# Performance work log

Measured on AMD Instinct MI355X. Metric: run time of the kernel, lower is better.

## Reference

```python
import math
import jax, jax.numpy as jnp
import numpy as np

B, N, T, H, DIN, NH = 4, 256, 30, 128, 3, 8
BN = B * N
DH = H // NH


def _pos_embed(t, h):
    pos = np.arange(t)[:, None].astype(np.float64)
    div = np.exp(np.arange(0, h, 2) * (-math.log(10000.0) / h))
    pe = np.zeros((t, h), np.float32)
    pe[:, 0::2] = np.sin(pos * div)
    pe[:, 1::2] = np.cos(pos * div)
    return jnp.asarray(pe)


def setup_inputs() -> dict:
    key = jax.random.key(0)
    ks = jax.random.split(key, 24)
    lin = lambda k, i, o: (jax.random.normal(k, (i, o), jnp.float32) / np.sqrt(i).astype(np.float32))
    vec = lambda k, o: jax.random.normal(k, (o,), jnp.float32) * 0.02
    return dict(
        x_raw=jax.random.normal(ks[0], (T, BN, DIN), jnp.float32),
        adjacency=jax.random.bernoulli(ks[1], 0.01, (T, BN, BN)).astype(jnp.float32),
        ego_mask=jax.random.bernoulli(ks[2], 0.5, (B, T, N)),
        W1=lin(ks[3], DIN, H), b1=vec(ks[4], H),
        W2=lin(ks[5], H, H), b2=vec(ks[6], H),
        Wq=lin(ks[7], H, H), bq=vec(ks[8], H),
        Wk=lin(ks[9], H, H), bk=vec(ks[10], H),
        Wv=lin(ks[11], H, H), bv=vec(ks[12], H),
        Wqi=lin(ks[13], H, H), bqi=vec(ks[14], H),
        Wki=lin(ks[15], H, H), bki=vec(ks[16], H),
        Wvi=lin(ks[17], H, H), bvi=vec(ks[18], H),
        Wo=lin(ks[19], H, H), bo=vec(ks[20], H),
    )


def reference(x_raw, adjacency, ego_mask,
              W1, b1, W2, b2,
              Wq, bq, Wk, bk, Wv, bv,
              Wqi, bqi, Wki, bki, Wvi, bvi,
              Wo, bo):
    # (B,T,N) -> (T, B*N) node-active mask, matching permute(1,0,2).reshape
    mask_flat = ego_mask.transpose(1, 0, 2).reshape(T, BN).astype(x_raw.dtype)

    def step(_, inp):
        x_t, A_t, m = inp  # (BN,DIN), (BN,BN), (BN,)
        # mask rows/cols (equiv. to gather A[idx][:,idx]) and add self loops
        A = A_t * m[:, None] * m[None, :] + jnp.diag(m)
        deg = A.sum(axis=1)
        dinv = jnp.where(deg > 0, 1.0, 0.0) * jax.lax.rsqrt(jnp.where(deg > 0, deg, 1.0))
        An = dinv[:, None] * A * dinv[None, :]  # D^-1/2 (A+I) D^-1/2
        h1 = jax.nn.relu(An @ (x_t @ W1) + b1)
        h2 = jax.nn.relu(An @ (h1 @ W2) + b2) * m[:, None]  # scatter back into zeros
        return None, h2

    _, hs = jax.lax.scan(step, None, (x_raw, adjacency, mask_flat))  # (T,BN,H)

    x_seq = hs.transpose(1, 0, 2) + _pos_embed(T, H)  # (BN,T,H)
    Q = x_seq @ Wq + bq
    K = x_seq @ Wk + bk
    V = x_seq @ Wv + bv
    # nn.MultiheadAttention applies its own in-projection to Q/K/V
    q = (Q @ Wqi + bqi).reshape(BN, T, NH, DH)
    k = (K @ Wki + bki).reshape(BN, T, NH, DH)
    v = (V @ Wvi + bvi).reshape(BN, T, NH, DH)
    attn = jax.nn.softmax(jnp.einsum('bthd,bshd->bhts', q, k) / np.sqrt(DH).astype(np.float32), axis=-1)
    o = jnp.einsum('bhts,bshd->bthd', attn, v).reshape(BN, T, H)
    out = (o @ Wo + bo).reshape(B, N, T, H)
    return out
```

## Files before the change

kernel.cpp:

```cpp
#include <hip/hip_runtime.h>
#include <hip/hip_bf16.h>
#include <math.h>

#define TT  30
#define BNN 1024
#define HH  128
#define MT  (TT*BNN)
#define CAP 64

typedef short bf16x8 __attribute__((ext_vector_type(8)));
typedef float f32x4 __attribute__((ext_vector_type(4)));

__device__ __forceinline__ float ldf(const void* p, size_t i, int fp) {
  if (fp == 0) {
    unsigned int w = ((unsigned int)(((const unsigned short*)p)[i])) << 16;
    float f; __builtin_memcpy(&f, &w, 4); return f;
  }
  return ((const float*)p)[i];
}
__device__ __forceinline__ float bf2f(unsigned short u) {
  unsigned int w = ((unsigned int)u) << 16;
  float f; __builtin_memcpy(&f, &w, 4); return f;
}
__device__ __forceinline__ unsigned short f2bf(float f) {
  unsigned int u; __builtin_memcpy(&u, &f, 4);
  return (unsigned short)((u + 0x7FFFu + ((u >> 16) & 1u)) >> 16);
}
__device__ __forceinline__ void splitbf(float a, unsigned short& h, unsigned short& l) {
  h = f2bf(a);
  l = f2bf(a - bf2f(h));
}

__global__ __launch_bounds__(1024) void detect_kernel(const unsigned char* xb, const unsigned char* eb, int* mode) {
  __shared__ int cnt_exp, f3F_odd1, f3F_any, fnz_notm4;
  int tid = threadIdx.x;
  if (tid == 0) { cnt_exp = 0; f3F_odd1 = 0; f3F_any = 0; fnz_notm4 = 0; }
  __syncthreads();
  int local = 0;
  for (int i = tid; i < 2048; i += 1024) {
    int e = (((const unsigned short*)xb)[i] >> 8) & 0x7F;
    if (e >= 0x3A && e <= 0x41) local++;
  }
  atomicAdd(&cnt_exp, local);
  int l1 = 0, l2 = 0, l3 = 0;
  for (int i = tid; i < 7680; i += 1024) {
    unsigned int w = ((const unsigned int*)eb)[i];
    #pragma unroll
    for (int e = 0; e < 4; ++e) {
      unsigned char b = (w >> (8 * e)) & 0xff;
      if (b == 0x3F) { l2 = 1; if (e == 1) l1 = 1; }
      if (b != 0 && e != 0) l3 = 1;
    }
  }
  if (l1) atomicOr(&f3F_odd1, 1);
  if (l2) atomicOr(&f3F_any, 1);
  if (l3) atomicOr(&fnz_notm4, 1);
  __syncthreads();
  if (tid == 0) {
    mode[0] = (cnt_exp > 1536) ? 0 : 1;
    mode[1] = f3F_odd1 ? 0 : (f3F_any ? 1 : (fnz_notm4 ? 2 : 3));
  }
}

__global__ __launch_bounds__(256) void setup_kernel(
    const void* ego,
    const void* W1, const void* b1, const void* W2, const void* b2, const void* Wo, const void* bo,
    const void* Wq, const void* bq, const void* Wk, const void* bk, const void* Wv, const void* bv,
    const void* Wqi, const void* bqi, const void* Wki, const void* bki, const void* Wvi, const void* bvi,
    const int* mode, float* pe, float* W1f, float* b1f, float* b2f, float* bof,
    unsigned short* W2h, unsigned short* W2l, unsigned short* Woh, unsigned short* Wol,
    unsigned short* Wch, unsigned short* Wcl, float* bqkv, float* maskf) {
  int bid = blockIdx.x;
  int fp = mode[0];
  if (bid < 15) {
    int idx = bid * 256 + threadIdx.x;
    if (idx >= TT * HH) return;
    int t = idx >> 7, i = idx & 127, j = i >> 1;
    double div = exp((double)(2 * j) * (-log(10000.0) / 128.0));
    double ang = (double)t * div;
    pe[idx] = (i & 1) ? (float)cos(ang) : (float)sin(ang);
    return;
  }
  if (bid < 146) {
    int idx = (bid - 15) * 256 + threadIdx.x;
    if (idx < 16384) { int k = idx >> 7, h = idx & 127; splitbf(ldf(W2, idx, fp), W2h[h * 128 + k], W2l[h * 128 + k]); return; }
    idx -= 16384;
    if (idx < 16384) { int k = idx >> 7, h = idx & 127; splitbf(ldf(Wo, idx, fp), Woh[h * 128 + k], Wol[h * 128 + k]); return; }
    idx -= 16384;
    if (idx < 384) { W1f[idx] = ldf(W1, idx, fp); return; } idx -= 384;
    if (idx < 128) { b1f[idx] = ldf(b1, idx, fp); return; } idx -= 128;
    if (idx < 128) { b2f[idx] = ldf(b2, idx, fp); return; } idx -= 128;
    if (idx < 128) { bof[idx] = ldf(bo, idx, fp); return; }
    return;
  }
  if (bid < 266) {
    int idx = (bid - 146) * 256 + threadIdx.x;
    if (idx >= MT) return;
    int t = idx >> 10, p = idx & 1023, b = p >> 8, n = p & 255;
    size_t e = (size_t)b * (TT * 256) + (size_t)t * 256 + n;
    int mm = mode[1];
    bool nz;
    if      (mm == 0) nz = ((const unsigned short*)ego)[e] != 0;
    else if (mm == 1) nz = ((const float*)ego)[e] != 0.f;
    else if (mm == 2) nz = ((const unsigned char*)ego)[e] != 0;
    else              nz = ((const int*)ego)[e] != 0;
    maskf[idx] = nz ? 1.f : 0.f;
    return;
  }
  int cb = bid - 266;
  int g = cb / 65;
  const void* Wa = (g == 0) ? Wq : (g == 1) ? Wk : Wv;
  const void* ba = (g == 0) ? bq : (g == 1) ? bk : bv;
  const void* Wb = (g == 0) ? Wqi : (g == 1) ? Wki : Wvi;
  const void* bb = (g == 0) ? bqi : (g == 1) ? bki : bvi;
  unsigned short* Wh = Wch + (size_t)g * 16384;
  unsigned short* Wl = Wcl + (size_t)g * 16384;
  float* bc = bqkv + g * 128;
  int idx = (cb % 65) * 256 + threadIdx.x;
  if (idx < 16384) {
    int k = idx >> 7, h = idx & 127;
    float s = 0.f;
    #pragma unroll 8
    for (int m = 0; m < 128; ++m) s += ldf(Wa, k * 128 + m, fp) * ldf(Wb, m * 128 + h, fp);
    splitbf(s, Wh[h * 128 + k], Wl[h * 128 + k]);
  } else if (idx < 16512) {
    int h = idx - 16384;
    float s = ldf(bb, h, fp);
    #pragma unroll 8
    for (int m = 0; m < 128; ++m) s += ldf(ba, m, fp) * ldf(Wb, m * 128 + h, fp);
    bc[h] = s;
  }
}

__global__ __launch_bounds__(256) void csr_kernel(const void* A, const int* mode, const float* maskf,
                                                  int* nnz, int* cols, float* dinv) {
  int fp = mode[0];
  int r = blockIdx.x * 4 + (threadIdx.x >> 6);
  int lane = threadIdx.x & 63;
  int t = r >> 10, i = r & 1023;
  int tb = t << 10;
  if (maskf[r] == 0.f) { if (lane == 0) { nnz[r] = 0; dinv[r] = 0.f; } return; }
  int* myc = cols + (size_t)r * CAP;
  int cnt = 0;
  unsigned long long lmask = (1ull << lane) - 1ull;
  if (fp == 1) {
    const float* Ar = (const float*)A + (size_t)t * BNN * BNN + (size_t)i * BNN;
    #pragma unroll
    for (int it = 0; it < 4; ++it) {
      int j0 = it * 256 + lane * 4;
      float4 av = *(const float4*)(Ar + j0);
      float4 mv = *(const float4*)(maskf + tb + j0);
      float va[4] = {av.x * mv.x, av.y * mv.y, av.z * mv.z, av.w * mv.w};
      #pragma unroll
      for (int e = 0; e < 4; ++e) {
        bool hit = va[e] != 0.f;
        unsigned long long bal = __ballot(hit);
        if (hit) { int pos = cnt + __popcll(bal & lmask); if (pos < CAP) myc[pos] = j0 + e; }
        cnt += __popcll(bal);
      }
    }
  } else {
    const unsigned short* Ar = (const unsigned short*)A + (size_t)t * BNN * BNN + (size_t)i * BNN;
    #pragma unroll
    for (int it = 0; it < 2; ++it) {
      int j0 = it * 512 + lane * 8;
      uint4 av = *(const uint4*)(Ar + j0);
      unsigned int wv[4] = {av.x, av.y, av.z, av.w};
      float4 m0 = *(const float4*)(maskf + tb + j0);
      float4 m1 = *(const float4*)(maskf + tb + j0 + 4);
      float mm[8] = {m0.x, m0.y, m0.z, m0.w, m1.x, m1.y, m1.z, m1.w};
      #pragma unroll
      for (int e = 0; e < 8; ++e) {
        unsigned short u = (wv[e >> 1] >> ((e & 1) * 16)) & 0xffff;
        bool hit = (u != 0) && (mm[e] != 0.f);
        unsigned long long bal = __ballot(hit);
        if (hit) { int pos = cnt + __popcll(bal & lmask); if (pos < CAP) myc[pos] = j0 + e; }
        cnt += __popcll(bal);
      }
    }
  }
  if (lane == 0) { nnz[r] = cnt > CAP ? CAP : cnt; dinv[r] = rsqrtf((float)cnt + 1.0f); }
}

__global__ __launch_bounds__(256) void spmm1_kernel(const void* x, const int* mode, const int* nnz,
    const int* cols, const float* dinv, const float* W1f, const float* b1f, float* h1) {
  int fp = mode[0];
  int r = blockIdx.x * 4 + (threadIdx.x >> 6);
  int lane = threadIdx.x & 63;
  int tbase = (r >> 10) << 10;
  int n = nnz[r];
  float s0 = 0.f, s1 = 0.f, s2 = 0.f;
  int j = -1;
  if (lane < n) j = tbase + cols[(size_t)r * CAP + lane];
  else if (lane == n) j = r;
  if (j >= 0) {
    float dj = dinv[j];
    s0 = dj * ldf(x, (size_t)j * 3 + 0, fp);
    s1 = dj * ldf(x, (size_t)j * 3 + 1, fp);
    s2 = dj * ldf(x, (size_t)j * 3 + 2, fp);
  }
  #pragma unroll
  for (int d = 1; d < 64; d <<= 1) {
    s0 += __shfl_xor(s0, d);
    s1 += __shfl_xor(s1, d);
    s2 += __shfl_xor(s2, d);
  }
  float dr = dinv[r];
  #pragma unroll
  for (int u = 0; u < 2; ++u) {
    int h = lane + u * 64;
    float v = dr * (s0 * W1f[h] + s1 * W1f[128 + h] + s2 * W1f[256 + h]) + b1f[h];
    h1[(size_t)r * 128 + h] = fmaxf(v, 0.f);
  }
}

__global__ __launch_bounds__(256) void spmm2_kernel(const float* g2s, const int* nnz, const int* cols,
    const float* dinv, const float* b2f, const float* maskf, const float* pe, float* xseq) {
  int r = blockIdx.x * 4 + (threadIdx.x >> 6);
  int lane = threadIdx.x & 63;
  int c = lane * 2;
  int t = r >> 10, i = r & 1023;
  int n = nnz[r];
  const int* myc = cols + (size_t)r * CAP;
  const float* st = g2s + ((size_t)(t << 10)) * 128;
  float2 acc = *(const float2*)(g2s + (size_t)r * 128 + c);
  for (int s = 0; s < n; ++s) {
    float2 v = *(const float2*)(st + (size_t)myc[s] * 128 + c);
    acc.x += v.x; acc.y += v.y;
  }
  float dr = dinv[r], m = maskf[r];
  float2 b = *(const float2*)(b2f + c);
  float2 p = *(const float2*)(pe + t * 128 + c);
  float vx = fmaxf(dr * acc.x + b.x, 0.f) * m + p.x;
  float vy = fmaxf(dr * acc.y + b.y, 0.f) * m + p.y;
  *(float2*)(xseq + ((size_t)i * TT + t) * 128 + c) = make_float2(vx, vy);
}

__global__ __launch_bounds__(256) void mfma_gemm(const float* A, const unsigned short* Bhi,
    const unsigned short* Blo, const float* scale, const float* bias,
    float* outf, void* outfin, const int* mode) {
  __shared__ __align__(16) unsigned short Ah[64 * 64];
  __shared__ __align__(16) unsigned short Al[64 * 64];
  __shared__ __align__(16) unsigned short Bh[128 * 64];
  __shared__ __align__(16) unsigned short Bl[128 * 64];
  int tid = threadIdx.x;
  int rowTile = blockIdx.x * 64;
  int gy = blockIdx.y;
  const unsigned short* Bhp = Bhi + (size_t)gy * 16384;
  const unsigned short* Blp = Blo + (size_t)gy * 16384;
  const float* bp = bias ? (bias + gy * 128) : nullptr;
  float* ofp = outf ? (outf + (size_t)gy * ((size_t)MT * 128)) : nullptr;

  int lane = tid & 63;
  int wid = tid >> 6;
  int wrow = (wid >> 1) * 32, wcol = (wid & 1) * 64;
  f32x4 acc[2][4];
  #pragma unroll
  for (int m = 0; m < 2; ++m)
    #pragma unroll
    for (int n = 0; n < 4; ++n) acc[m][n] = (f32x4){0.f, 0.f, 0.f, 0.f};

  for (int kb = 0; kb < 2; ++kb) {
    __syncthreads();
    #pragma unroll
    for (int it = 0; it < 2; ++it) {
      int c = it * 256 + tid;
      int r = c >> 3, cc = c & 7;
      int swz = (cc ^ (r & 7)) * 16;
      const float* ap = A + (size_t)(rowTile + r) * 128 + kb * 64 + cc * 8;
      float4 f0 = *(const float4*)ap;
      float4 f1 = *(const float4*)(ap + 4);
      float fa[8] = {f0.x, f0.y, f0.z, f0.w, f1.x, f1.y, f1.z, f1.w};
      unsigned short hi[8], lo[8];
      #pragma unroll
      for (int e = 0; e < 8; ++e) splitbf(fa[e], hi[e], lo[e]);
      uint4 ph, pl;
      ph.x = hi[0] | ((unsigned)hi[1] << 16); ph.y = hi[2] | ((unsigned)hi[3] << 16);
      ph.z = hi[4] | ((unsigned)hi[5] << 16); ph.w = hi[6] | ((unsigned)hi[7] << 16);
      pl.x = lo[0] | ((unsigned)lo[1] << 16); pl.y = lo[2] | ((unsigned)lo[3] << 16);
      pl.z = lo[4] | ((unsigned)lo[5] << 16); pl.w = lo[6] | ((unsigned)lo[7] << 16);
      *(uint4*)((char*)Ah + r * 128 + swz) = ph;
      *(uint4*)((char*)Al + r * 128 + swz) = pl;
    }
    #pragma unroll
    for (int it = 0; it < 4; ++it) {
      int c = it * 256 + tid;
      int r = c >> 3, cc = c & 7;
      int swz = (cc ^ (r & 7)) * 16;
      *(uint4*)((char*)Bh + r * 128 + swz) = *(const uint4*)(Bhp + (size_t)r * 128 + kb * 64 + cc * 8);
      *(uint4*)((char*)Bl + r * 128 + swz) = *(const uint4*)(Blp + (size_t)r * 128 + kb * 64 + cc * 8);
    }
    __syncthreads();
    #pragma unroll
    for (int ks = 0; ks < 2; ++ks) {
      bf16x8 ah[2], al[2], bh[4], bl[4];
      #pragma unroll
      for (int m = 0; m < 2; ++m) {
        int R = wrow + m * 16 + (lane & 15);
        int cc = ks * 4 + (lane >> 4);
        int off = R * 128 + ((cc ^ (R & 7)) * 16);
        ah[m] = *(const bf16x8*)((const char*)Ah + off);
        al[m] = *(const bf16x8*)((const char*)Al + off);
      }
      #pragma unroll
      for (int n = 0; n < 4; ++n) {
        int R = wcol + n * 16 + (lane & 15);
        int cc = ks * 4 + (lane >> 4);
        int off = R * 128 + ((cc ^ (R & 7)) * 16);
        bh[n] = *(const bf16x8*)((const char*)Bh + off);
        bl[n] = *(const bf16x8*)((const char*)Bl + off);
      }
      #pragma unroll
      for (int m = 0; m < 2; ++m)
        #pragma unroll
        for (int n = 0; n < 4; ++n) {
          acc[m][n] = __builtin_amdgcn_mfma_f32_16x16x32_bf16(ah[m], bl[n], acc[m][n], 0, 0, 0);
          acc[m][n] = __builtin_amdgcn_mfma_f32_16x16x32_bf16(al[m], bh[n], acc[m][n], 0, 0, 0);
          acc[m][n] = __builtin_amdgcn_mfma_f32_16x16x32_bf16(ah[m], bh[n], acc[m][n], 0, 0, 0);
        }
    }
  }
  int fp = mode[0];
  #pragma unroll
  for (int m = 0; m < 2; ++m) {
    #pragma unroll
    for (int n = 0; n < 4; ++n) {
      int col = wcol + n * 16 + (lane & 15);
      float bv = bp ? bp[col] : 0.f;
      #pragma unroll
      for (int q = 0; q < 4; ++q) {
        int row = rowTile + wrow + m * 16 + (lane >> 4) * 4 + q;
        float v = acc[m][n][q];
        if (scale) v *= scale[row];
        v += bv;
        size_t o = (size_t)row * 128 + col;
        if (ofp)           ofp[o] = v;
        else if (fp == 0)  ((unsigned short*)outfin)[o] = f2bf(v);
        else               ((float*)outfin)[o] = v;
      }
    }
  }
}

__global__ __launch_bounds__(256) void attn_kernel(const float* Q, const float* K, const float* V, float* O) {
  __shared__ __align__(16) float ksm[TT * 128];
  __shared__ __align__(16) float vsm[TT * 128];
  int tid = threadIdx.x;
  size_t base = (size_t)blockIdx.x * (TT * 128);
  for (int i = tid; i < TT * 128 / 4; i += 256) {
    ((float4*)ksm)[i] = ((const float4*)(K + base))[i];
    ((float4*)vsm)[i] = ((const float4*)(V + base))[i];
  }
  int h = tid >> 5, t = tid & 31;
  float q[16];
  if (t < TT) {
    const float4* qp = (const float4*)(Q + base + (size_t)t * 128 + h * 16);
    #pragma unroll
    for (int e = 0; e < 4; ++e) { float4 f = qp[e]; q[4*e] = f.x; q[4*e+1] = f.y; q[4*e+2] = f.z; q[4*e+3] = f.w; }
  }
  __syncthreads();
  if (t >= TT) return;
  float p[TT];
  float mx = -1e30f;
  #pragma unroll
  for (int s = 0; s < TT; ++s) {
    const float4* kp = (const float4*)&ksm[s * 128 + h * 16];
    float d = 0.f;
    #pragma unroll
    for (int e = 0; e < 4; ++e) {
      float4 f = kp[e];
      d += q[4*e] * f.x + q[4*e+1] * f.y + q[4*e+2] * f.z + q[4*e+3] * f.w;
    }
    p[s] = d * 0.25f;
    mx = fmaxf(mx, p[s]);
  }
  float sum = 0.f;
  #pragma unroll
  for (int s = 0; s < TT; ++s) { p[s] = __expf(p[s] - mx); sum += p[s]; }
  float inv = 1.f / sum;
  float o[16];
  #pragma unroll
  for (int e = 0; e < 16; ++e) o[e] = 0.f;
  #pragma unroll
  for (int s = 0; s < TT; ++s) {
    const float4* vp = (const float4*)&vsm[s * 128 + h * 16];
    float ps = p[s] * inv;
    #pragma unroll
    for (int e = 0; e < 4; ++e) {
      float4 f = vp[e];
      o[4*e] += ps * f.x; o[4*e+1] += ps * f.y; o[4*e+2] += ps * f.z; o[4*e+3] += ps * f.w;
    }
  }
  float* op = O + base + (size_t)t * 128 + h * 16;
  #pragma unroll
  for (int e = 0; e < 4; ++e)
    ((float4*)op)[e] = make_float4(o[4*e], o[4*e+1], o[4*e+2], o[4*e+3]);
}

extern "C" void kernel_launch(void* const* d_in, const int* in_sizes, int n_in,
                              void* d_out, int out_size, void* d_ws, size_t ws_size,
                              hipStream_t stream) {
  (void)in_sizes; (void)n_in; (void)out_size;
  const void* x_raw = d_in[0];
  const void* adj   = d_in[1];
  const void* ego   = d_in[2];
  const void* W1 = d_in[3];  const void* b1 = d_in[4];
  const void* W2 = d_in[5];  const void* b2 = d_in[6];
  const void* Wq = d_in[7];  const void* bq = d_in[8];
  const void* Wk = d_in[9];  const void* bk = d_in[10];
  const void* Wv = d_in[11]; const void* bv = d_in[12];
  const void* Wqi = d_in[13]; const void* bqi = d_in[14];
  const void* Wki = d_in[15]; const void* bki = d_in[16];
  const void* Wvi = d_in[17]; const void* bvi = d_in[18];
  const void* Wo = d_in[19]; const void* bo = d_in[20];

  char* w = (char*)d_ws;
  auto alloc = [&](size_t b) { char* p = w; w += (b + 255) & ~(size_t)255; return p; };
  int*   mode  = (int*)  alloc(16);
  float* maskf = (float*)alloc((size_t)MT * 4);
  float* dinv  = (float*)alloc((size_t)MT * 4);
  float* pe    = (float*)alloc((size_t)TT * HH * 4);
  float* W1f   = (float*)alloc(384 * 4);
  float* b1f   = (float*)alloc(128 * 4);
  float* b2f   = (float*)alloc(128 * 4);
  float* bof   = (float*)alloc(128 * 4);
  unsigned short* W2h = (unsigned short*)alloc(16384 * 2);
  unsigned short* W2l = (unsigned short*)alloc(16384 * 2);
  unsigned short* Woh = (unsigned short*)alloc(16384 * 2);
  unsigned short* Wol = (unsigned short*)alloc(16384 * 2);
  unsigned short* Wch = (unsigned short*)alloc((size_t)3 * 16384 * 2);
  unsigned short* Wcl = (unsigned short*)alloc((size_t)3 * 16384 * 2);
  float* bqkv  = (float*)alloc(3 * 128 * 4);
  int*   nnz   = (int*)  alloc((size_t)MT * 4);
  int*   cols  = (int*)  alloc((size_t)MT * CAP * 4);
  float* h1    = (float*)alloc((size_t)MT * 128 * 4);
  float* g2s   = (float*)alloc((size_t)MT * 128 * 4);
  float* xseq  = (float*)alloc((size_t)MT * 128 * 4);
  float* qkv   = (float*)alloc((size_t)3 * MT * 128 * 4);
  float* ob    = (float*)alloc((size_t)MT * 128 * 4);
  size_t need = (size_t)(w - (char*)d_ws);
  if (need > ws_size) return;

  detect_kernel<<<1, 1024, 0, stream>>>((const unsigned char*)x_raw, (const unsigned char*)ego, mode);
  setup_kernel<<<461, 256, 0, stream>>>(ego, W1, b1, W2, b2, Wo, bo,
                                        Wq, bq, Wk, bk, Wv, bv, Wqi, bqi, Wki, bki, Wvi, bvi,
                                        mode, pe, W1f, b1f, b2f, bof,
                                        W2h, W2l, Woh, Wol, Wch, Wcl, bqkv, maskf);
  csr_kernel<<<MT / 4, 256, 0, stream>>>(adj, mode, maskf, nnz, cols, dinv);
  spmm1_kernel<<<MT / 4, 256, 0, stream>>>(x_raw, mode, nnz, cols, dinv, W1f, b1f, h1);
  mfma_gemm<<<480, 256, 0, stream>>>(h1, W2h, W2l, dinv, nullptr, g2s, nullptr, mode);
  spmm2_kernel<<<MT / 4, 256, 0, stream>>>(g2s, nnz, cols, dinv, b2f, maskf, pe, xseq);
  mfma_gemm<<<dim3(480, 3), 256, 0, stream>>>(xseq, Wch, Wcl, nullptr, bqkv, qkv, nullptr, mode);
  attn_kernel<<<BNN, 256, 0, stream>>>(qkv, qkv + (size_t)MT * 128, qkv + (size_t)2 * MT * 128, ob);
  mfma_gemm<<<480, 256, 0, stream>>>(ob, Woh, Wol, nullptr, bof, nullptr, d_out, mode);
}
```

Baseline: 133.1 us.

## Pre-split GEMM A operands to bf16 hi/lo in producers, merge detect into setup

The producer kernels (spmm1, spmm2, attention) now write their outputs directly as bf16 hi/lo pairs, so the MFMA GEMM loads ready-made bf16 tiles instead of converting fp32 A tiles on every load. The QKV GEMM now loops over the three weight groups inside one block, reusing the A-tile rows rather than launching a 3-wide grid. The separate detect kernel is folded into setup_kernel, where each block recomputes the dtype detection locally, which saves one launch but adds redundant detection work per block.

```diff
diff --git a/kernel.cpp b/kernel.cpp
--- a/kernel.cpp
+++ b/kernel.cpp
@@ -31,20 +31,26 @@
   l = f2bf(a - bf2f(h));
 }
 
-__global__ __launch_bounds__(1024) void detect_kernel(const unsigned char* xb, const unsigned char* eb, int* mode) {
-  __shared__ int cnt_exp, f3F_odd1, f3F_any, fnz_notm4;
-  int tid = threadIdx.x;
-  if (tid == 0) { cnt_exp = 0; f3F_odd1 = 0; f3F_any = 0; fnz_notm4 = 0; }
+__device__ int block_detect_fp(const unsigned short* xw) {
+  __shared__ int cnt_exp;
+  if (threadIdx.x == 0) cnt_exp = 0;
   __syncthreads();
   int local = 0;
-  for (int i = tid; i < 2048; i += 1024) {
-    int e = (((const unsigned short*)xb)[i] >> 8) & 0x7F;
+  for (int i = threadIdx.x; i < 2048; i += 256) {
+    int e = (xw[i] >> 8) & 0x7F;
     if (e >= 0x3A && e <= 0x41) local++;
   }
   atomicAdd(&cnt_exp, local);
+  __syncthreads();
+  return (cnt_exp > 1536) ? 0 : 1;
+}
+__device__ int block_detect_ego(const unsigned int* ew) {
+  __shared__ int f_odd1, f_any, f_nz;
+  if (threadIdx.x == 0) { f_odd1 = 0; f_any = 0; f_nz = 0; }
+  __syncthreads();
   int l1 = 0, l2 = 0, l3 = 0;
-  for (int i = tid; i < 7680; i += 1024) {
-    unsigned int w = ((const unsigned int*)eb)[i];
+  for (int i = threadIdx.x; i < 7680; i += 256) {
+    unsigned int w = ew[i];
     #pragma unroll
     for (int e = 0; e < 4; ++e) {
       unsigned char b = (w >> (8 * e)) & 0xff;
@@ -52,37 +58,39 @@
       if (b != 0 && e != 0) l3 = 1;
     }
   }
-  if (l1) atomicOr(&f3F_odd1, 1);
-  if (l2) atomicOr(&f3F_any, 1);
-  if (l3) atomicOr(&fnz_notm4, 1);
+  if (l1) atomicOr(&f_odd1, 1);
+  if (l2) atomicOr(&f_any, 1);
+  if (l3) atomicOr(&f_nz, 1);
   __syncthreads();
-  if (tid == 0) {
-    mode[0] = (cnt_exp > 1536) ? 0 : 1;
-    mode[1] = f3F_odd1 ? 0 : (f3F_any ? 1 : (fnz_notm4 ? 2 : 3));
-  }
+  return f_odd1 ? 0 : (f_any ? 1 : (f_nz ? 2 : 3));
 }
 
 __global__ __launch_bounds__(256) void setup_kernel(
-    const void* ego,
+    const void* x_raw, const void* ego,
     const void* W1, const void* b1, const void* W2, const void* b2, const void* Wo, const void* bo,
     const void* Wq, const void* bq, const void* Wk, const void* bk, const void* Wv, const void* bv,
     const void* Wqi, const void* bqi, const void* Wki, const void* bki, const void* Wvi, const void* bvi,
-    const int* mode, float* pe, float* W1f, float* b1f, float* b2f, float* bof,
+    int* mode, float* pe, float* W1f, float* b1f, float* b2f, float* bof,
     unsigned short* W2h, unsigned short* W2l, unsigned short* Woh, unsigned short* Wol,
     unsigned short* Wch, unsigned short* Wcl, float* bqkv, float* maskf) {
   int bid = blockIdx.x;
-  int fp = mode[0];
-  if (bid < 15) {
-    int idx = bid * 256 + threadIdx.x;
-    if (idx >= TT * HH) return;
+  if (bid == 0) {
+    int fp = block_detect_fp((const unsigned short*)x_raw);
+    int mm = block_detect_ego((const unsigned int*)ego);
+    if (threadIdx.x == 0) { mode[0] = fp; mode[1] = mm; }
+    return;
+  }
+  if (bid < 16) {
+    int idx = (bid - 1) * 256 + threadIdx.x;
     int t = idx >> 7, i = idx & 127, j = i >> 1;
     double div = exp((double)(2 * j) * (-log(10000.0) / 128.0));
     double ang = (double)t * div;
     pe[idx] = (i & 1) ? (float)cos(ang) : (float)sin(ang);
     return;
   }
-  if (bid < 146) {
-    int idx = (bid - 15) * 256 + threadIdx.x;
+  if (bid < 147) {
+    int fp = block_detect_fp((const unsigned short*)x_raw);
+    int idx = (bid - 16) * 256 + threadIdx.x;
     if (idx < 16384) { int k = idx >> 7, h = idx & 127; splitbf(ldf(W2, idx, fp), W2h[h * 128 + k], W2l[h * 128 + k]); return; }
     idx -= 16384;
     if (idx < 16384) { int k = idx >> 7, h = idx & 127; splitbf(ldf(Wo, idx, fp), Woh[h * 128 + k], Wol[h * 128 + k]); return; }
@@ -93,12 +101,11 @@
     if (idx < 128) { bof[idx] = ldf(bo, idx, fp); return; }
     return;
   }
-  if (bid < 266) {
-    int idx = (bid - 146) * 256 + threadIdx.x;
-    if (idx >= MT) return;
+  if (bid < 267) {
+    int mm = block_detect_ego((const unsigned int*)ego);
+    int idx = (bid - 147) * 256 + threadIdx.x;
     int t = idx >> 10, p = idx & 1023, b = p >> 8, n = p & 255;
     size_t e = (size_t)b * (TT * 256) + (size_t)t * 256 + n;
-    int mm = mode[1];
     bool nz;
     if      (mm == 0) nz = ((const unsigned short*)ego)[e] != 0;
     else if (mm == 1) nz = ((const float*)ego)[e] != 0.f;
@@ -107,7 +114,8 @@
     maskf[idx] = nz ? 1.f : 0.f;
     return;
   }
-  int cb = bid - 266;
+  int fp = block_detect_fp((const unsigned short*)x_raw);
+  int cb = bid - 267;
   int g = cb / 65;
   const void* Wa = (g == 0) ? Wq : (g == 1) ? Wk : Wv;
   const void* ba = (g == 0) ? bq : (g == 1) ? bk : bv;
@@ -183,7 +191,8 @@
 }
 
 __global__ __launch_bounds__(256) void spmm1_kernel(const void* x, const int* mode, const int* nnz,
-    const int* cols, const float* dinv, const float* W1f, const float* b1f, float* h1) {
+    const int* cols, const float* dinv, const float* W1f, const float* b1f,
+    unsigned short* h1h, unsigned short* h1l) {
   int fp = mode[0];
   int r = blockIdx.x * 4 + (threadIdx.x >> 6);
   int lane = threadIdx.x & 63;
@@ -210,12 +219,13 @@
   for (int u = 0; u < 2; ++u) {
     int h = lane + u * 64;
     float v = dr * (s0 * W1f[h] + s1 * W1f[128 + h] + s2 * W1f[256 + h]) + b1f[h];
-    h1[(size_t)r * 128 + h] = fmaxf(v, 0.f);
+    splitbf(fmaxf(v, 0.f), h1h[(size_t)r * 128 + h], h1l[(size_t)r * 128 + h]);
   }
 }
 
 __global__ __launch_bounds__(256) void spmm2_kernel(const float* g2s, const int* nnz, const int* cols,
-    const float* dinv, const float* b2f, const float* maskf, const float* pe, float* xseq) {
+    const float* dinv, const float* b2f, const float* maskf, const float* pe,
+    unsigned short* xh, unsigned short* xl) {
   int r = blockIdx.x * 4 + (threadIdx.x >> 6);
   int lane = threadIdx.x & 63;
   int c = lane * 2;
@@ -233,116 +243,109 @@
   float2 p = *(const float2*)(pe + t * 128 + c);
   float vx = fmaxf(dr * acc.x + b.x, 0.f) * m + p.x;
   float vy = fmaxf(dr * acc.y + b.y, 0.f) * m + p.y;
-  *(float2*)(xseq + ((size_t)i * TT + t) * 128 + c) = make_float2(vx, vy);
-}
-
-__global__ __launch_bounds__(256) void mfma_gemm(const float* A, const unsigned short* Bhi,
-    const unsigned short* Blo, const float* scale, const float* bias,
-    float* outf, void* outfin, const int* mode) {
+  size_t o = ((size_t)i * TT + t) * 128 + c;
+  splitbf(vx, xh[o], xl[o]);
+  splitbf(vy, xh[o + 1], xl[o + 1]);
+}
+
+__global__ __launch_bounds__(256) void mfma_gemm(const unsigned short* Ahi, const unsigned short* Alo,
+    const unsigned short* Bhi, const unsigned short* Blo, int ng,
+    const float* scale, const float* bias, float* outf, void* outfin, const int* mode) {
   __shared__ __align__(16) unsigned short Ah[64 * 64];
   __shared__ __align__(16) unsigned short Al[64 * 64];
   __shared__ __align__(16) unsigned short Bh[128 * 64];
   __shared__ __align__(16) unsigned short Bl[128 * 64];
   int tid = threadIdx.x;
   int rowTile = blockIdx.x * 64;
-  int gy = blockIdx.y;
-  const unsigned short* Bhp = Bhi + (size_t)gy * 16384;
-  const unsigned short* Blp = Blo + (size_t)gy * 16384;
-  const float* bp = bias ? (bias + gy * 128) : nullptr;
-  float* ofp = outf ? (outf + (size_t)gy * ((size_t)MT * 128)) : nullptr;
-
   int lane = tid & 63;
   int wid = tid >> 6;
   int wrow = (wid >> 1) * 32, wcol = (wid & 1) * 64;
-  f32x4 acc[2][4];
-  #pragma unroll
-  for (int m = 0; m < 2; ++m)
-    #pragma unroll
-    for (int n = 0; n < 4; ++n) acc[m][n] = (f32x4){0.f, 0.f, 0.f, 0.f};
-
-  for (int kb = 0; kb < 2; ++kb) {
-    __syncthreads();
-    #pragma unroll
-    for (int it = 0; it < 2; ++it) {
-      int c = it * 256 + tid;
-      int r = c >> 3, cc = c & 7;
-      int swz = (cc ^ (r & 7)) * 16;
-      const float* ap = A + (size_t)(rowTile + r) * 128 + kb * 64 + cc * 8;
-      float4 f0 = *(const float4*)ap;
-      float4 f1 = *(const float4*)(ap + 4);
-      float fa[8] = {f0.x, f0.y, f0.z, f0.w, f1.x, f1.y, f1.z, f1.w};
-      unsigned short hi[8], lo[8];
-      #pragma unroll
-      for (int e = 0; e < 8; ++e) splitbf(fa[e], hi[e], lo[e]);
-      uint4 ph, pl;
-      ph.x = hi[0] | ((unsigned)hi[1] << 16); ph.y = hi[2] | ((unsigned)hi[3] << 16);
-      ph.z = hi[4] | ((unsigned)hi[5] << 16); ph.w = hi[6] | ((unsigned)hi[7] << 16);
-      pl.x = lo[0] | ((unsigned)lo[1] << 16); pl.y = lo[2] | ((unsigned)lo[3] << 16);
-      pl.z = lo[4] | ((unsigned)lo[5] << 16); pl.w = lo[6] | ((unsigned)lo[7] << 16);
-      *(uint4*)((char*)Ah + r * 128 + swz) = ph;
-      *(uint4*)((char*)Al + r * 128 + swz) = pl;
-    }
-    #pragma unroll
-    for (int it = 0; it < 4; ++it) {
-      int c = it * 256 + tid;
-      int r = c >> 3, cc = c & 7;
-      int swz = (cc ^ (r & 7)) * 16;
-      *(uint4*)((char*)Bh + r * 128 + swz) = *(const uint4*)(Bhp + (size_t)r * 128 + kb * 64 + cc * 8);
-      *(uint4*)((char*)Bl + r * 128 + swz) = *(const uint4*)(Blp + (size_t)r * 128 + kb * 64 + cc * 8);
-    }
-    __syncthreads();
-    #pragma unroll
-    for (int ks = 0; ks < 2; ++ks) {
-      bf16x8 ah[2], al[2], bh[4], bl[4];
-      #pragma unroll
-      for (int m = 0; m < 2; ++m) {
-        int R = wrow + m * 16 + (lane & 15);
-        int cc = ks * 4 + (lane >> 4);
-        int off = R * 128 + ((cc ^ (R & 7)) * 16);
-        ah[m] = *(const bf16x8*)((const char*)Ah + off);
-        al[m] = *(const bf16x8*)((const char*)Al + off);
-      }
-      #pragma unroll
-      for (int n = 0; n < 4; ++n) {
-        int R = wcol + n * 16 + (lane & 15);
-        int cc = ks * 4 + (lane >> 4);
-        int off = R * 128 + ((cc ^ (R & 7)) * 16);
-        bh[n] = *(const bf16x8*)((const char*)Bh + off);
-        bl[n] = *(const bf16x8*)((const char*)Bl + off);
-      }
-      #pragma unroll
-      for (int m = 0; m < 2; ++m)
+  int fp = mode[0];
+
+  for (int g = 0; g < ng; ++g) {
+    const unsigned short* Bhp = Bhi + (size_t)g * 16384;
+    const unsigned short* Blp = Blo + (size_t)g * 16384;
+    f32x4 acc[2][4];
+    #pragma unroll
+    for (int m = 0; m < 2; ++m)
+      #pragma unroll
+      for (int n = 0; n < 4; ++n) acc[m][n] = (f32x4){0.f, 0.f, 0.f, 0.f};
+
+    for (int kb = 0; kb < 2; ++kb) {
+      __syncthreads();
+      #pragma unroll
+      for (int it = 0; it < 2; ++it) {
+        int c = it * 256 + tid;
+        int r = c >> 3, cc = c & 7;
+        int swz = (cc ^ (r & 7)) * 16;
+        size_t src = (size_t)(rowTile + r) * 128 + kb * 64 + cc * 8;
+        *(uint4*)((char*)Ah + r * 128 + swz) = *(const uint4*)(Ahi + src);
+        *(uint4*)((char*)Al + r * 128 + swz) = *(const uint4*)(Alo + src);
+      }
+      #pragma unroll
+      for (int it = 0; it < 4; ++it) {
+        int c = it * 256 + tid;
+        int r = c >> 3, cc = c & 7;
+        int swz = (cc ^ (r & 7)) * 16;
+        *(uint4*)((char*)Bh + r * 128 + swz) = *(const uint4*)(Bhp + (size_t)r * 128 + kb * 64 + cc * 8);
+        *(uint4*)((char*)Bl + r * 128 + swz) = *(const uint4*)(Blp + (size_t)r * 128 + kb * 64 + cc * 8);
+      }
+      __syncthreads();
+      #pragma unroll
+      for (int ks = 0; ks < 2; ++ks) {
+        bf16x8 ah[2], al[2], bh[4], bl[4];
+        #pragma unroll
+        for (int m = 0; m < 2; ++m) {
+          int R = wrow + m * 16 + (lane & 15);
+          int cc = ks * 4 + (lane >> 4);
+          int off = R * 128 + ((cc ^ (R & 7)) * 16);
+          ah[m] = *(const bf16x8*)((const char*)Ah + off);
+          al[m] = *(const bf16x8*)((const char*)Al + off);
+        }
         #pragma unroll
         for (int n = 0; n < 4; ++n) {
-          acc[m][n] = __builtin_amdgcn_mfma_f32_16x16x32_bf16(ah[m], bl[n], acc[m][n], 0, 0, 0);
-          acc[m][n] = __builtin_amdgcn_mfma_f32_16x16x32_bf16(al[m], bh[n], acc[m][n], 0, 0, 0);
-          acc[m][n] = __builtin_amdgcn_mfma_f32_16x16x32_bf16(ah[m], bh[n], acc[m][n], 0, 0, 0);
+          int R = wcol + n * 16 + (lane & 15);
+          int cc = ks * 4 + (lane >> 4);
+          int off = R * 128 + ((cc ^ (R & 7)) * 16);
+          bh[n] = *(const bf16x8*)((const char*)Bh + off);
+          bl[n] = *(const bf16x8*)((const char*)Bl + off);
         }
-    }
-  }
-  int fp = mode[0];
-  #pragma unroll
-  for (int m = 0; m < 2; ++m) {
-    #pragma unroll
-    for (int n = 0; n < 4; ++n) {
-      int col = wcol + n * 16 + (lane & 15);
-      float bv = bp ? bp[col] : 0.f;
-      #pragma unroll
-      for (int q = 0; q < 4; ++q) {
-        int row = rowTile + wrow + m * 16 + (lane >> 4) * 4 + q;
-        float v = acc[m][n][q];
-        if (scale) v *= scale[row];
-        v += bv;
-        size_t o = (size_t)row * 128 + col;
-        if (ofp)           ofp[o] = v;
-        else if (fp == 0)  ((unsigned short*)outfin)[o] = f2bf(v);
-        else               ((float*)outfin)[o] = v;
-      }
-    }
-  }
-}
-
-__global__ __launch_bounds__(256) void attn_kernel(const float* Q, const float* K, const float* V, float* O) {
+        #pragma unroll
+        for (int m = 0; m < 2; ++m)
+          #pragma unroll
+          for (int n = 0; n < 4; ++n) {
+            acc[m][n] = __builtin_amdgcn_mfma_f32_16x16x32_bf16(ah[m], bl[n], acc[m][n], 0, 0, 0);
+            acc[m][n] = __builtin_amdgcn_mfma_f32_16x16x32_bf16(al[m], bh[n], acc[m][n], 0, 0, 0);
+            acc[m][n] = __builtin_amdgcn_mfma_f32_16x16x32_bf16(ah[m], bh[n], acc[m][n], 0, 0, 0);
+          }
+      }
+    }
+    const float* bp = bias ? (bias + g * 128) : nullptr;
+    float* ofp = outf ? (outf + (size_t)g * ((size_t)MT * 128)) : nullptr;
+    #pragma unroll
+    for (int m = 0; m < 2; ++m) {
+      #pragma unroll
+      for (int n = 0; n < 4; ++n) {
+        int col = wcol + n * 16 + (lane & 15);
+        float bv = bp ? bp[col] : 0.f;
+        #pragma unroll
+        for (int q = 0; q < 4; ++q) {
+          int row = rowTile + wrow + m * 16 + (lane >> 4) * 4 + q;
+          float v = acc[m][n][q];
+          if (scale) v *= scale[row];
+          v += bv;
+          size_t o = (size_t)row * 128 + col;
+          if (ofp)           ofp[o] = v;
+          else if (fp == 0)  ((unsigned short*)outfin)[o] = f2bf(v);
+          else               ((float*)outfin)[o] = v;
+        }
+      }
+    }
+  }
+}
+
+__global__ __launch_bounds__(256) void attn_kernel(const float* Q, const float* K, const float* V,
+                                                   unsigned short* obh, unsigned short* obl) {
   __shared__ __align__(16) float ksm[TT * 128];
   __shared__ __align__(16) float vsm[TT * 128];
   int tid = threadIdx.x;
@@ -391,10 +394,21 @@
       o[4*e] += ps * f.x; o[4*e+1] += ps * f.y; o[4*e+2] += ps * f.z; o[4*e+3] += ps * f.w;
     }
   }
-  float* op = O + base + (size_t)t * 128 + h * 16;
-  #pragma unroll
-  for (int e = 0; e < 4; ++e)
-    ((float4*)op)[e] = make_float4(o[4*e], o[4*e+1], o[4*e+2], o[4*e+3]);
+  unsigned short hi[16], lo[16];
+  #pragma unroll
+  for (int e = 0; e < 16; ++e) splitbf(o[e], hi[e], lo[e]);
+  size_t oo = base + (size_t)t * 128 + h * 16;
+  uint4 ph0, ph1, pl0, pl1;
+  ph0.x = hi[0] | ((unsigned)hi[1] << 16);  ph0.y = hi[2] | ((unsigned)hi[3] << 16);
+  ph0.z = hi[4] | ((unsigned)hi[5] << 16);  ph0.w = hi[6] | ((unsigned)hi[7] << 16);
+  ph1.x = hi[8] | ((unsigned)hi[9] << 16);  ph1.y = hi[10] | ((unsigned)hi[11] << 16);
+  ph1.z = hi[12] | ((unsigned)hi[13] << 16); ph1.w = hi[14] | ((unsigned)hi[15] << 16);
+  pl0.x = lo[0] | ((unsigned)lo[1] << 16);  pl0.y = lo[2] | ((unsigned)lo[3] << 16);
+  pl0.z = lo[4] | ((unsigned)lo[5] << 16);  pl0.w = lo[6] | ((unsigned)lo[7] << 16);
+  pl1.x = lo[8] | ((unsigned)lo[9] << 16);  pl1.y = lo[10] | ((unsigned)lo[11] << 16);
+  pl1.z = lo[12] | ((unsigned)lo[13] << 16); pl1.w = lo[14] | ((unsigned)lo[15] << 16);
+  *(uint4*)(obh + oo) = ph0; *(uint4*)(obh + oo + 8) = ph1;
+  *(uint4*)(obl + oo) = pl0; *(uint4*)(obl + oo + 8) = pl1;
 }
 
 extern "C" void kernel_launch(void* const* d_in, const int* in_sizes, int n_in,
@@ -433,24 +447,26 @@
   float* bqkv  = (float*)alloc(3 * 128 * 4);
   int*   nnz   = (int*)  alloc((size_t)MT * 4);
   int*   cols  = (int*)  alloc((size_t)MT * CAP * 4);
-  float* h1    = (float*)alloc((size_t)MT * 128 * 4);
+  unsigned short* h1h = (unsigned short*)alloc((size_t)MT * 128 * 2);
+  unsigned short* h1l = (unsigned short*)alloc((size_t)MT * 128 * 2);
+  unsigned short* xh  = (unsigned short*)alloc((size_t)MT * 128 * 2);
+  unsigned short* xl  = (unsigned short*)alloc((size_t)MT * 128 * 2);
+  unsigned short* obh = (unsigned short*)alloc((size_t)MT * 128 * 2);
+  unsigned short* obl = (unsigned short*)alloc((size_t)MT * 128 * 2);
   float* g2s   = (float*)alloc((size_t)MT * 128 * 4);
-  float* xseq  = (float*)alloc((size_t)MT * 128 * 4);
   float* qkv   = (float*)alloc((size_t)3 * MT * 128 * 4);
-  float* ob    = (float*)alloc((size_t)MT * 128 * 4);
   size_t need = (size_t)(w - (char*)d_ws);
   if (need > ws_size) return;
 
-  detect_kernel<<<1, 1024, 0, stream>>>((const unsigned char*)x_raw, (const unsigned char*)ego, mode);
-  setup_kernel<<<461, 256, 0, stream>>>(ego, W1, b1, W2, b2, Wo, bo,
+  setup_kernel<<<462, 256, 0, stream>>>(x_raw, ego, W1, b1, W2, b2, Wo, bo,
                                         Wq, bq, Wk, bk, Wv, bv, Wqi, bqi, Wki, bki, Wvi, bvi,
                                         mode, pe, W1f, b1f, b2f, bof,
                                         W2h, W2l, Woh, Wol, Wch, Wcl, bqkv, maskf);
   csr_kernel<<<MT / 4, 256, 0, stream>>>(adj, mode, maskf, nnz, cols, dinv);
-  spmm1_kernel<<<MT / 4, 256, 0, stream>>>(x_raw, mode, nnz, cols, dinv, W1f, b1f, h1);
-  mfma_gemm<<<480, 256, 0, stream>>>(h1, W2h, W2l, dinv, nullptr, g2s, nullptr, mode);
-  spmm2_kernel<<<MT / 4, 256, 0, stream>>>(g2s, nnz, cols, dinv, b2f, maskf, pe, xseq);
-  mfma_gemm<<<dim3(480, 3), 256, 0, stream>>>(xseq, Wch, Wcl, nullptr, bqkv, qkv, nullptr, mode);
-  attn_kernel<<<BNN, 256, 0, stream>>>(qkv, qkv + (size_t)MT * 128, qkv + (size_t)2 * MT * 128, ob);
-  mfma_gemm<<<480, 256, 0, stream>>>(ob, Woh, Wol, nullptr, bof, nullptr, d_out, mode);
-}
+  spmm1_kernel<<<MT / 4, 256, 0, stream>>>(x_raw, mode, nnz, cols, dinv, W1f, b1f, h1h, h1l);
+  mfma_gemm<<<480, 256, 0, stream>>>(h1h, h1l, W2h, W2l, 1, dinv, nullptr, g2s, nullptr, mode);
+  spmm2_kernel<<<MT / 4, 256, 0, stream>>>(g2s, nnz, cols, dinv, b2f, maskf, pe, xh, xl);
+  mfma_gemm<<<480, 256, 0, stream>>>(xh, xl, Wch, Wcl, 3, nullptr, bqkv, qkv, nullptr, mode);
+  attn_kernel<<<BNN, 256, 0, stream>>>(qkv, qkv + (size_t)MT * 128, qkv + (size_t)2 * MT * 128, obh, obl);
+  mfma_gemm<<<480, 256, 0, stream>>>(obh, obl, Woh, Wol, 1, nullptr, bof, nullptr, d_out, mode);
+}
```

New measurement: 152.3 us. 1.14x slower.
